# Performance work log

Hardware: AMD Instinct MI355X
Metric: run time of the kernel (lower is better)

## Reference

```python
import jax, jax.numpy as jnp
import numpy as np

D = 1024      # atrybuty (d_model)
H = 16        # kanaly (heads)
DH = D // H   # head dim
B, T = 4, 2048
EPS = 1e-5


def setup_inputs() -> dict:
    key = jax.random.key(0)
    ks = jax.random.split(key, 16)
    s = 0.02
    return {
        "x":  jax.random.normal(ks[0], (B, T, D), jnp.float32),
        "wq": jax.random.normal(ks[1], (D, D), jnp.float32) * s,
        "wk": jax.random.normal(ks[2], (D, D), jnp.float32) * s,
        "wv": jax.random.normal(ks[3], (D, D), jnp.float32) * s,
        "wp": jax.random.normal(ks[4], (D, D), jnp.float32) * s,
        "bp": jnp.zeros((D,), jnp.float32),
        "w1": jax.random.normal(ks[5], (D, 4 * D), jnp.float32) * s,
        "b1": jnp.zeros((4 * D,), jnp.float32),
        "w2": jax.random.normal(ks[6], (4 * D, D), jnp.float32) * s,
        "b2": jnp.zeros((D,), jnp.float32),
        "g1": jnp.ones((D,), jnp.float32),
        "be1": jnp.zeros((D,), jnp.float32),
        "g2": jnp.ones((D,), jnp.float32),
        "be2": jnp.zeros((D,), jnp.float32),
    }


def _layernorm(x, g, b):
    mu = jnp.mean(x, axis=-1, keepdims=True)
    var = jnp.mean(jnp.square(x - mu), axis=-1, keepdims=True)
    return (x - mu) * jax.lax.rsqrt(var + EPS) * g + b


def reference(x, wq, wk, wv, wp, bp, w1, b1, w2, b2, g1, be1, g2, be2):
    b, t, d = x.shape
    # --- self-attention on ln1(x) ---
    h = _layernorm(x, g1, be1)
    # per-head Linears are equivalent to one [D,D] projection split into heads
    q = (h @ wq).reshape(b, t, H, DH).transpose(0, 2, 1, 3)  # [B,H,T,Dh]
    k = (h @ wk).reshape(b, t, H, DH).transpose(0, 2, 1, 3)
    v = (h @ wv).reshape(b, t, H, DH).transpose(0, 2, 1, 3)
    # NOTE: original scales by full embed dim C, not head_dim
    scale = jnp.asarray(d, x.dtype) ** -0.5
    wei = jnp.einsum("bhqd,bhkd->bhqk", q, k) * scale
    causal = jnp.tril(jnp.ones((t, t), bool))
    wei = jnp.where(causal, wei, -jnp.inf)
    wei = jax.nn.softmax(wei, axis=-1)
    att = jnp.einsum("bhqk,bhkd->bhqd", wei, v)
    att = att.transpose(0, 2, 1, 3).reshape(b, t, d)
    x = x + att @ wp + bp
    # --- feedforward on ln2(x) ---
    h2 = _layernorm(x, g2, be2)
    x = x + jax.nn.relu(h2 @ w1 + b1) @ w2 + b2
    return x
```

## Files before the change

kernel.cpp:

```cpp
#include <hip/hip_runtime.h>
#include <hip/hip_bf16.h>
#include <stdint.h>

#define DM   1024
#define NH   16
#define DH   64
#define BATCH 4
#define SEQ  2048
#define MROWS (BATCH*SEQ)

typedef float f32x4 __attribute__((ext_vector_type(4)));
typedef __bf16 bf16x8 __attribute__((ext_vector_type(8)));
typedef short s16x4 __attribute__((ext_vector_type(4)));
typedef int   i32x2 __attribute__((ext_vector_type(2)));

#define QSCALE 0.045084220f

#define VM(n) asm volatile("s_waitcnt vmcnt(" #n ")" ::: "memory")
#define LGKM0 do { asm volatile("s_waitcnt lgkmcnt(0)" ::: "memory"); \
                   __builtin_amdgcn_sched_barrier(0); } while (0)

__device__ __forceinline__ short f2bs(float f) {
    __bf16 h = (__bf16)f;
    return __builtin_bit_cast(short, h);
}

__device__ __forceinline__ void gload_lds16(const void* g, void* l) {
    __builtin_amdgcn_global_load_lds(
        (__attribute__((address_space(1))) void*)(g),
        (__attribute__((address_space(3))) void*)(l), 16, 0, 0);
}

__device__ __forceinline__ void swz_xy(int ny, int& x, int& y) {
    const int bid = blockIdx.x;
    const int cpx = gridDim.x >> 3;
    const int wg  = (bid & 7) * cpx + (bid >> 3);
    x = wg / ny;
    y = wg % ny;
}

__global__ __launch_bounds__(256) void transpose_cvt_kernel(
    const float* __restrict__ w, short* __restrict__ wt, int K, int N)
{
    __shared__ short tile[64 * 65];
    const int k0 = blockIdx.x * 64, n0 = blockIdx.y * 64;
    const int t = threadIdx.x;
#pragma unroll
    for (int i = 0; i < 16; ++i) {
        int idx = i * 256 + t;
        int r = idx >> 6, c = idx & 63;
        tile[r * 65 + c] = f2bs(w[(size_t)(k0 + r) * N + n0 + c]);
    }
    __syncthreads();
#pragma unroll
    for (int i = 0; i < 16; ++i) {
        int idx = i * 256 + t;
        int r = idx >> 6, c = idx & 63;
        wt[(size_t)(n0 + r) * K + k0 + c] = tile[c * 65 + r];
    }
}

__global__ __launch_bounds__(256) void ln_kernel(
    const float* __restrict__ x, const float* __restrict__ g,
    const float* __restrict__ be, short* __restrict__ out)
{
    const int row = blockIdx.x, t = threadIdx.x;
    const float4 v = ((const float4*)(x + (size_t)row * DM))[t];
    float s  = v.x + v.y + v.z + v.w;
    float ss = v.x * v.x + v.y * v.y + v.z * v.z + v.w * v.w;
#pragma unroll
    for (int d = 1; d < 64; d <<= 1) {
        s  += __shfl_xor(s, d, 64);
        ss += __shfl_xor(ss, d, 64);
    }
    __shared__ float red[8];
    const int wid = t >> 6;
    if ((t & 63) == 0) { red[wid] = s; red[wid + 4] = ss; }
    __syncthreads();
    s  = red[0] + red[1] + red[2] + red[3];
    ss = red[4] + red[5] + red[6] + red[7];
    const float mu = s * (1.0f / DM);
    const float rs = rsqrtf(ss * (1.0f / DM) - mu * mu + 1e-5f);
    const float4 gg = ((const float4*)g)[t];
    const float4 bb = ((const float4*)be)[t];
    short4 o;
    o.x = f2bs((v.x - mu) * rs * gg.x + bb.x);
    o.y = f2bs((v.y - mu) * rs * gg.y + bb.y);
    o.z = f2bs((v.z - mu) * rs * gg.z + bb.z);
    o.w = f2bs((v.w - mu) * rs * gg.w + bb.w);
    ((short4*)(out + (size_t)row * DM))[t] = o;
}

template<int NCHUNK>
__device__ __forceinline__ void stage32(
    const short* __restrict__ G, int ldk, int row0, int k0,
    short* __restrict__ lds, int t)
{
#pragma unroll
    for (int i = 0; i < NCHUNK / 512; ++i) {
        const int c  = i * 512 + t;
        const int r  = c >> 2;
        const int sl = (c & 3) ^ ((r >> 1) & 3);
        gload_lds16(&G[(size_t)(row0 + r) * ldk + k0 + sl * 8], &lds[c * 8]);
    }
}

template<int EPI>
__global__ __launch_bounds__(512) void gemm256(
    const short* __restrict__ A, const short* __restrict__ Bt,
    int N, int K, int nyT,
    const float* __restrict__ bias, short* __restrict__ outb,
    short* __restrict__ qo, short* __restrict__ ko, short* __restrict__ vo)
{
    __shared__ short As[4][8192];
    __shared__ short Bs[4][8192];
    const int t = threadIdx.x, lane = t & 63, w = t >> 6;
    const int l15 = lane & 15, hi = lane >> 4;
    const int wm = (w >> 2) * 128, wn = (w & 3) * 64;
    int bx, by; swz_xy(nyT, bx, by);
    const int m0 = bx * 256, n0 = by * 256;
    const int NT = K >> 5;

    f32x4 acc[8][4] = {};

    stage32<1024>(A, K, m0, 0,  As[0], t); stage32<1024>(Bt, K, n0, 0,  Bs[0], t);
    stage32<1024>(A, K, m0, 32, As[1], t); stage32<1024>(Bt, K, n0, 32, Bs[1], t);
    stage32<1024>(A, K, m0, 64, As[2], t); stage32<1024>(Bt, K, n0, 64, Bs[2], t);
    VM(8);
    __builtin_amdgcn_s_barrier();

    for (int kt = 0; kt < NT; ++kt) {
        const short* Ac = As[kt & 3];
        const short* Bc = Bs[kt & 3];
        const int k3 = (kt + 3) << 5;
        bf16x8 af[8], bfr[4];

#pragma unroll
        for (int fm = 0; fm < 4; ++fm) {
            const int r = wm + fm * 16 + l15;
            af[fm] = *(const bf16x8*)&Ac[r * 32 + ((hi ^ ((r >> 1) & 3)) << 3)];
        }
#pragma unroll
        for (int fn = 0; fn < 4; ++fn) {
            const int r = wn + fn * 16 + l15;
            bfr[fn] = *(const bf16x8*)&Bc[r * 32 + ((hi ^ ((r >> 1) & 3)) << 3)];
        }
        if (kt + 3 < NT) stage32<1024>(A, K, m0, k3, As[(kt + 3) & 3], t);
        __builtin_amdgcn_s_barrier();
        LGKM0;
        __builtin_amdgcn_s_setprio(1);
#pragma unroll
        for (int fm = 0; fm < 4; ++fm)
#pragma unroll
            for (int fn = 0; fn < 4; ++fn)
                acc[fm][fn] = __builtin_amdgcn_mfma_f32_16x16x32_bf16(
                    af[fm], bfr[fn], acc[fm][fn], 0, 0, 0);
        __builtin_amdgcn_s_setprio(0);
        __builtin_amdgcn_s_barrier();

#pragma unroll
        for (int fm = 4; fm < 8; ++fm) {
            const int r = wm + fm * 16 + l15;
            af[fm] = *(const bf16x8*)&Ac[r * 32 + ((hi ^ ((r >> 1) & 3)) << 3)];
        }
        if (kt + 3 < NT) {
            stage32<1024>(Bt, K, n0, k3, Bs[(kt + 3) & 3], t);
            VM(8);
        } else if (kt + 2 < NT) VM(4);
        else if (kt + 1 < NT) VM(0);
        __builtin_amdgcn_s_barrier();
        LGKM0;
        __builtin_amdgcn_s_setprio(1);
#pragma unroll
        for (int fm = 4; fm < 8; ++fm)
#pragma unroll
            for (int fn = 0; fn < 4; ++fn)
                acc[fm][fn] = __builtin_amdgcn_mfma_f32_16x16x32_bf16(
                    af[fm], bfr[fn], acc[fm][fn], 0, 0, 0);
        __builtin_amdgcn_s_setprio(0);
        __builtin_amdgcn_s_barrier();
    }

#pragma unroll
    for (int fm = 0; fm < 8; ++fm)
#pragma unroll
        for (int fn = 0; fn < 4; ++fn) {
            const int row0 = m0 + wm + fm * 16 + hi * 4;
            const int nn = n0 + wn + fn * 16 + l15;
            const f32x4 a = acc[fm][fn];
            if constexpr (EPI == 0) {
                const int mat = nn >> 10, n1 = nn & 1023;
                const int head = n1 >> 6, dh = n1 & 63;
                if (mat == 2) {
                    const int tok = row0 & 2047, b = row0 >> 11;
                    const int tokp = (tok & ~63) |
                        (((((tok >> 3) & 7) ^ (dh & 7)) << 3)) | (tok & 7);
                    short4 pk;
                    pk.x = f2bs(a[0]); pk.y = f2bs(a[1]);
                    pk.z = f2bs(a[2]); pk.w = f2bs(a[3]);
                    *(short4*)&vo[((size_t)(b * NH + head) * DH + dh) * SEQ + tokp] = pk;
                } else if (mat == 1) {
#pragma unroll
                    for (int rr = 0; rr < 4; ++rr) {
                        const int m = row0 + rr;
                        const int b = m >> 11, tok = m & 2047;
                        const int dhp = (((dh >> 3) ^ (tok & 7)) << 3) | (dh & 7);
                        ko[((size_t)(b * NH + head) * SEQ + tok) * DH + dhp] =
                            f2bs(a[rr]);
                    }
                } else {
#pragma unroll
                    for (int rr = 0; rr < 4; ++rr) {
                        const int m = row0 + rr;
                        const int b = m >> 11, tok = m & 2047;
                        qo[((size_t)(b * NH + head) * SEQ + tok) * DH + dh] =
                            f2bs(a[rr] * QSCALE);
                    }
                }
            } else {
                const float bb = bias[nn];
#pragma unroll
                for (int rr = 0; rr < 4; ++rr) {
                    const float z = a[rr] + bb;
                    outb[(size_t)(row0 + rr) * N + nn] = f2bs(z > 0.f ? z : 0.f);
                }
            }
        }
}

__global__ __launch_bounds__(512) void gemm128n(
    const short* __restrict__ A, const short* __restrict__ Bt,
    int N, int K, int nyT,
    const float* __restrict__ bias, const float* __restrict__ res,
    float* __restrict__ outf)
{
    __shared__ short As[4][8192];
    __shared__ short Bs[4][4096];
    const int t = threadIdx.x, lane = t & 63, w = t >> 6;
    const int l15 = lane & 15, hi = lane >> 4;
    const int wm = (w >> 1) * 64, wn = (w & 1) * 64;
    int bx, by; swz_xy(nyT, bx, by);
    const int m0 = bx * 256, n0 = by * 128;
    const int NT = K >> 5;

    f32x4 acc[4][4] = {};

    stage32<1024>(A, K, m0, 0,  As[0], t); stage32<512>(Bt, K, n0, 0,  Bs[0], t);
    stage32<1024>(A, K, m0, 32, As[1], t); stage32<512>(Bt, K, n0, 32, Bs[1], t);
    stage32<1024>(A, K, m0, 64, As[2], t); stage32<512>(Bt, K, n0, 64, Bs[2], t);

    for (int kt = 0; kt < NT; ++kt) {
        if (kt + 3 < NT) {
            stage32<1024>(A,  K, m0, (kt + 3) << 5, As[(kt + 3) & 3], t);
            stage32<512>(Bt, K, n0, (kt + 3) << 5, Bs[(kt + 3) & 3], t);
            VM(9);
        } else if (kt + 2 < NT) VM(6);
        else if (kt + 1 < NT) VM(3);
        else VM(0);
        __builtin_amdgcn_s_barrier();

        const short* Ac = As[kt & 3];
        const short* Bc = Bs[kt & 3];
        bf16x8 af[4], bfr[4];
#pragma unroll
        for (int fm = 0; fm < 4; ++fm) {
            const int r = wm + fm * 16 + l15;
            af[fm] = *(const bf16x8*)&Ac[r * 32 + ((hi ^ ((r >> 1) & 3)) << 3)];
        }
#pragma unroll
        for (int fn = 0; fn < 4; ++fn) {
            const int r = wn + fn * 16 + l15;
            bfr[fn] = *(const bf16x8*)&Bc[r * 32 + ((hi ^ ((r >> 1) & 3)) << 3)];
        }
        LGKM0;
        __builtin_amdgcn_s_barrier();

        __builtin_amdgcn_s_setprio(1);
#pragma unroll
        for (int fm = 0; fm < 4; ++fm)
#pragma unroll
            for (int fn = 0; fn < 4; ++fn)
                acc[fm][fn] = __builtin_amdgcn_mfma_f32_16x16x32_bf16(
                    af[fm], bfr[fn], acc[fm][fn], 0, 0, 0);
        __builtin_amdgcn_s_setprio(0);
    }

#pragma unroll
    for (int fm = 0; fm < 4; ++fm)
#pragma unroll
        for (int fn = 0; fn < 4; ++fn) {
            const int row0 = m0 + wm + fm * 16 + hi * 4;
            const int nn = n0 + wn + fn * 16 + l15;
            const float bb = bias[nn];
            const f32x4 a = acc[fm][fn];
#pragma unroll
            for (int rr = 0; rr < 4; ++rr) {
                const int m = row0 + rr;
                outf[(size_t)m * N + nn] = a[rr] + bb + res[(size_t)m * N + nn];
            }
        }
}

__global__ __launch_bounds__(128) void attn_kernel(
    const short* __restrict__ Q, const short* __restrict__ Kx,
    const short* __restrict__ Vt, short* __restrict__ att)
{
    __shared__ short Ks[2][4096];
    __shared__ short Vs[2][4096];

    const int n  = blockIdx.x;
    const int bh = n & 63;
    const int qi = 31 - (n >> 6);
    const int tid = threadIdx.x;
    const int wv = tid >> 6;
    const int lane = tid & 63;
    const int l15 = lane & 15, hi = lane >> 4;
    const int q0 = qi * 64;
    const int qw = q0 + wv * 32;
    const size_t base  = (size_t)bh * (SEQ * DH);
    const size_t vbase = (size_t)bh * (DH * SEQ);
    const int b = bh >> 4, head = bh & 15;

    bf16x8 qf[2][2];
#pragma unroll
    for (int mf = 0; mf < 2; ++mf)
#pragma unroll
        for (int kf = 0; kf < 2; ++kf)
            qf[mf][kf] = *(const bf16x8*)
                &Q[base + (size_t)(qw + mf * 16 + l15) * DH + kf * 32 + hi * 8];

    f32x4 O[2][4] = {};
    float L[2] = {0.f, 0.f};

    const int nkv = qi + 1;

#define STAGE_KV(TT, BUF)                                                      \
    do {                                                                       \
        const int kvo = (TT) * 64;                                             \
        _Pragma("unroll")                                                      \
        for (int i2 = 0; i2 < 4; ++i2) {                                       \
            const int c = i2 * 128 + tid;                                      \
            const int rw = c >> 3, sl = c & 7;                                 \
            gload_lds16(&Kx[base + (size_t)(kvo + rw) * DH + sl * 8],          \
                        &Ks[BUF][c * 8]);                                      \
            gload_lds16(&Vt[vbase + (size_t)rw * SEQ + kvo + sl * 8],          \
                        &Vs[BUF][c * 8]);                                      \
        }                                                                      \
    } while (0)

    STAGE_KV(0, 0);

    for (int t2 = 0; t2 < nkv; ++t2) {
        if (t2 + 1 < nkv) { STAGE_KV(t2 + 1, (t2 + 1) & 1); VM(8); }
        else VM(0);
        __builtin_amdgcn_s_barrier();
        __builtin_amdgcn_sched_barrier(0);

        const short* Kc = Ks[t2 & 1];
        const short* Vc = Vs[t2 & 1];
        const int kv0 = t2 * 64;

        bf16x8 kfr[4][2];
#pragma unroll
        for (int nf = 0; nf < 4; ++nf)
#pragma unroll
            for (int kf = 0; kf < 2; ++kf)
                kfr[nf][kf] = *(const bf16x8*)
                    &Kc[(nf * 16 + l15) * 64 + (((kf * 4 + hi) ^ (l15 & 7)) << 3)];

        f32x4 St[4][2] = {};
#pragma unroll
        for (int kf = 0; kf < 2; ++kf)
#pragma unroll
            for (int nf = 0; nf < 4; ++nf)
#pragma unroll
                for (int mf = 0; mf < 2; ++mf)
                    St[nf][mf] = __builtin_amdgcn_mfma_f32_16x16x32_bf16(
                        kfr[nf][kf], qf[mf][kf], St[nf][mf], 0, 0, 0);

        if (kv0 + 63 > qw) {
#pragma unroll
            for (int mf = 0; mf < 2; ++mf) {
                const int q = qw + mf * 16 + l15;
#pragma unroll
                for (int nf = 0; nf < 4; ++nf)
#pragma unroll
                    for (int r = 0; r < 4; ++r) {
                        const int kv = kv0 + nf * 16 + hi * 4 + r;
                        if (kv > q) St[nf][mf][r] = -3.0e38f;
                    }
            }
        }

        s16x4 pa[4][2];
#pragma unroll
        for (int nf = 0; nf < 4; ++nf)
#pragma unroll
            for (int mf = 0; mf < 2; ++mf) {
                const float p0 = exp2f(St[nf][mf][0]);
                const float p1 = exp2f(St[nf][mf][1]);
                const float p2 = exp2f(St[nf][mf][2]);
                const float p3 = exp2f(St[nf][mf][3]);
                L[mf] += (p0 + p1) + (p2 + p3);
                unsigned dw0, dw1;
                asm("v_cvt_pk_bf16_f32 %0, %1, %2" : "=v"(dw0) : "v"(p0), "v"(p1));
                asm("v_cvt_pk_bf16_f32 %0, %1, %2" : "=v"(dw1) : "v"(p2), "v"(p3));
                i32x2 dd; dd[0] = (int)dw0; dd[1] = (int)dw1;
                pa[nf][mf] = __builtin_bit_cast(s16x4, dd);
            }

#pragma unroll
        for (int nf = 0; nf < 4; ++nf)
#pragma unroll
            for (int jf = 0; jf < 4; ++jf) {
                const s16x4 vfr = *(const s16x4*)
                    &Vc[(jf * 16 + l15) * 64 +
                        ((((nf * 2 + (hi >> 1)) ^ (l15 & 7)) << 3) + ((hi & 1) << 2))];
#pragma unroll
                for (int mf = 0; mf < 2; ++mf)
                    O[mf][jf] = __builtin_amdgcn_mfma_f32_16x16x16bf16_1k(
                        pa[nf][mf], vfr, O[mf][jf], 0, 0, 0);
            }

        __builtin_amdgcn_sched_barrier(0);
        __builtin_amdgcn_s_barrier();
    }
#undef STAGE_KV

#pragma unroll
    for (int mf = 0; mf < 2; ++mf) {
        L[mf] += __shfl_xor(L[mf], 16, 64);
        L[mf] += __shfl_xor(L[mf], 32, 64);
    }
    const float inv0 = 1.0f / L[0], inv1 = 1.0f / L[1];

#pragma unroll
    for (int mf = 0; mf < 2; ++mf) {
        const float invm = mf ? inv1 : inv0;
#pragma unroll
        for (int r = 0; r < 4; ++r) {
            const int addr = ((lane >> 4) << 4) + (r << 2);
            const float iv = __builtin_bit_cast(float,
                __builtin_amdgcn_ds_bpermute(addr, __builtin_bit_cast(int, invm)));
            const int q = qw + mf * 16 + hi * 4 + r;
#pragma unroll
            for (int jf = 0; jf < 4; ++jf)
                att[(size_t)(b * SEQ + q) * DM + head * DH + jf * 16 + l15] =
                    f2bs(O[mf][jf][r] * iv);
        }
    }
}

extern "C" void kernel_launch(void* const* d_in, const int* in_sizes, int n_in,
                              void* d_out, int out_size, void* d_ws, size_t ws_size,
                              hipStream_t stream) {
    const float* x   = (const float*)d_in[0];
    const float* wq  = (const float*)d_in[1];
    const float* wk  = (const float*)d_in[2];
    const float* wv  = (const float*)d_in[3];
    const float* wp  = (const float*)d_in[4];
    const float* bp  = (const float*)d_in[5];
    const float* w1  = (const float*)d_in[6];
    const float* b1  = (const float*)d_in[7];
    const float* w2  = (const float*)d_in[8];
    const float* b2  = (const float*)d_in[9];
    const float* g1  = (const float*)d_in[10];
    const float* be1 = (const float*)d_in[11];
    const float* g2  = (const float*)d_in[12];
    const float* be2 = (const float*)d_in[13];
    float* out = (float*)d_out;

    char* ws = (char*)d_ws;
    short* wqkv_t = (short*)(ws + 0);
    short* wp_t   = (short*)(ws + 6291456);
    short* w1_t   = (short*)(ws + 8388608);
    short* w2_t   = (short*)(ws + 16777216);
    short* h      = (short*)(ws + 25165824);
    short* qb     = (short*)(ws + 41943040);
    short* kb     = (short*)(ws + 58720256);
    short* vb     = (short*)(ws + 75497472);
    short* att    = (short*)(ws + 92274688);
    float* x1     = (float*)(ws + 109051904);
    short* h2     = (short*)(ws + 142606336);
    short* tbuf   = (short*)(ws + 25165824);

    dim3 blk(256);

    transpose_cvt_kernel<<<dim3(16, 16), blk, 0, stream>>>(wq, wqkv_t,                1024, 1024);
    transpose_cvt_kernel<<<dim3(16, 16), blk, 0, stream>>>(wk, wqkv_t + 1024 * 1024,  1024, 1024);
    transpose_cvt_kernel<<<dim3(16, 16), blk, 0, stream>>>(wv, wqkv_t + 2048 * 1024,  1024, 1024);
    transpose_cvt_kernel<<<dim3(16, 16), blk, 0, stream>>>(wp, wp_t,                  1024, 1024);
    transpose_cvt_kernel<<<dim3(16, 64), blk, 0, stream>>>(w1, w1_t,                  1024, 4096);
    transpose_cvt_kernel<<<dim3(64, 16), blk, 0, stream>>>(w2, w2_t,                  4096, 1024);

    ln_kernel<<<MROWS, blk, 0, stream>>>(x, g1, be1, h);

    gemm256<0><<<dim3(384), dim3(512), 0, stream>>>(h, wqkv_t, 3072, 1024, 12,
        nullptr, nullptr, qb, kb, vb);

    attn_kernel<<<dim3(2048), dim3(128), 0, stream>>>(qb, kb, vb, att);

    gemm128n<<<dim3(256), dim3(512), 0, stream>>>(att, wp_t, 1024, 1024, 8,
        bp, x, x1);

    ln_kernel<<<MROWS, blk, 0, stream>>>(x1, g2, be2, h2);

    gemm256<2><<<dim3(512), dim3(512), 0, stream>>>(h2, w1_t, 4096, 1024, 16,
        b1, tbuf, nullptr, nullptr, nullptr);

    gemm128n<<<dim3(256), dim3(512), 0, stream>>>(tbuf, w2_t, 1024, 4096, 8,
        b2, x1, out);
}
```

Before: 421.7 us.

## Shrink N=1024 output GEMMs to 128x128 tiles with double-buffered LDS

The output-projection and FFN down-projection GEMMs move from a 256x128 tile with 8 waves and a 4-stage LDS ring to a 128x128 tile with 4 waves and a 2-stage ring. The grid grows from 256 to 512 blocks. That fills the GPU's compute units more evenly and lowers LDS use per block, which could let more blocks fit per CU. In exchange, each tile reuses less data, and the shallower prefetch exposes more global-load latency.

```diff
diff --git a/kernel.cpp b/kernel.cpp
--- a/kernel.cpp
+++ b/kernel.cpp
@@ -228,39 +228,50 @@
         }
 }
 
-__global__ __launch_bounds__(512) void gemm128n(
+__global__ __launch_bounds__(256) void gemm_bt128(
     const short* __restrict__ A, const short* __restrict__ Bt,
     int N, int K, int nyT,
     const float* __restrict__ bias, const float* __restrict__ res,
     float* __restrict__ outf)
 {
-    __shared__ short As[4][8192];
-    __shared__ short Bs[4][4096];
+    __shared__ short As[2][4096];
+    __shared__ short Bs[2][4096];
     const int t = threadIdx.x, lane = t & 63, w = t >> 6;
     const int l15 = lane & 15, hi = lane >> 4;
-    const int wm = (w >> 1) * 64, wn = (w & 1) * 64;
+    const int wm = (w & 1) * 64, wn = (w >> 1) * 64;
     int bx, by; swz_xy(nyT, bx, by);
-    const int m0 = bx * 256, n0 = by * 128;
+    const int m0 = bx * 128, n0 = by * 128;
     const int NT = K >> 5;
 
     f32x4 acc[4][4] = {};
 
-    stage32<1024>(A, K, m0, 0,  As[0], t); stage32<512>(Bt, K, n0, 0,  Bs[0], t);
-    stage32<1024>(A, K, m0, 32, As[1], t); stage32<512>(Bt, K, n0, 32, Bs[1], t);
-    stage32<1024>(A, K, m0, 64, As[2], t); stage32<512>(Bt, K, n0, 64, Bs[2], t);
+#define STAGE128(G, row0, k0, lds)                                            \
+    do {                                                                      \
+        _Pragma("unroll")                                                     \
+        for (int i2 = 0; i2 < 2; ++i2) {                                      \
+            const int c  = i2 * 256 + t;                                      \
+            const int r  = c >> 2;                                            \
+            const int sl = (c & 3) ^ ((r >> 1) & 3);                          \
+            gload_lds16(&(G)[(size_t)((row0) + r) * K + (k0) + sl * 8],       \
+                        &(lds)[c * 8]);                                       \
+        }                                                                     \
+    } while (0)
+
+    STAGE128(A, m0, 0, As[0]);
+    STAGE128(Bt, n0, 0, Bs[0]);
 
     for (int kt = 0; kt < NT; ++kt) {
-        if (kt + 3 < NT) {
-            stage32<1024>(A,  K, m0, (kt + 3) << 5, As[(kt + 3) & 3], t);
-            stage32<512>(Bt, K, n0, (kt + 3) << 5, Bs[(kt + 3) & 3], t);
-            VM(9);
-        } else if (kt + 2 < NT) VM(6);
-        else if (kt + 1 < NT) VM(3);
-        else VM(0);
-        __builtin_amdgcn_s_barrier();
-
-        const short* Ac = As[kt & 3];
-        const short* Bc = Bs[kt & 3];
+        if (kt + 1 < NT) {
+            STAGE128(A, m0, (kt + 1) << 5, As[(kt + 1) & 1]);
+            STAGE128(Bt, n0, (kt + 1) << 5, Bs[(kt + 1) & 1]);
+            VM(4);
+        } else {
+            VM(0);
+        }
+        __builtin_amdgcn_s_barrier();
+
+        const short* Ac = As[kt & 1];
+        const short* Bc = Bs[kt & 1];
         bf16x8 af[4], bfr[4];
 #pragma unroll
         for (int fm = 0; fm < 4; ++fm) {
@@ -284,6 +295,7 @@
                     af[fm], bfr[fn], acc[fm][fn], 0, 0, 0);
         __builtin_amdgcn_s_setprio(0);
     }
+#undef STAGE128
 
 #pragma unroll
     for (int fm = 0; fm < 4; ++fm)
@@ -500,7 +512,7 @@
 
     attn_kernel<<<dim3(2048), dim3(128), 0, stream>>>(qb, kb, vb, att);
 
-    gemm128n<<<dim3(256), dim3(512), 0, stream>>>(att, wp_t, 1024, 1024, 8,
+    gemm_bt128<<<dim3(512), blk, 0, stream>>>(att, wp_t, 1024, 1024, 8,
         bp, x, x1);
 
     ln_kernel<<<MROWS, blk, 0, stream>>>(x1, g2, be2, h2);
@@ -508,6 +520,6 @@
     gemm256<2><<<dim3(512), dim3(512), 0, stream>>>(h2, w1_t, 4096, 1024, 16,
         b1, tbuf, nullptr, nullptr, nullptr);
 
-    gemm128n<<<dim3(256), dim3(512), 0, stream>>>(tbuf, w2_t, 1024, 4096, 8,
+    gemm_bt128<<<dim3(512), blk, 0, stream>>>(tbuf, w2_t, 1024, 4096, 8,
         b2, x1, out);
 }
```

Measured after the change: 395.5 us. -6.2%, faster.
